# Kernel optimization log

Measured on AMD Instinct MI355X. Metric: run time of the kernel, lower is better.

## Reference

```python
import jax, jax.numpy as jnp
import numpy as np

B, N, DIM, C_IN, C_OUT = 2, 512, 3, 64, 64


def setup_inputs() -> dict:
    key = jax.random.key(0)
    ks = jax.random.split(key, 9)
    geom = jax.random.normal(ks[0], (B, N, DIM, C_IN), dtype=jnp.float32)
    adj = jax.random.uniform(ks[1], (B, N, N, 1, 1), dtype=jnp.float32)
    rel = jax.random.normal(ks[2], (B, N, N, DIM, 1), dtype=jnp.float32)
    emb = jax.random.normal(ks[3], (B, N, N, 1), dtype=jnp.float32)
    # learned parameters
    theta = jax.random.normal(ks[4], (C_IN + 1, C_OUT), dtype=jnp.float32) * 0.1
    norm_w = jax.random.normal(ks[5], (C_IN + 1, 1), dtype=jnp.float32) * 0.1
    norm_b = jax.random.normal(ks[6], (1,), dtype=jnp.float32) * 0.1
    alpha = jax.random.normal(ks[7], (1, 1, C_OUT), dtype=jnp.float32) * 0.1
    beta = jax.random.normal(ks[8], (1, 1, C_OUT), dtype=jnp.float32) * 0.1
    return {
        "geometric_information": geom,
        "adjacency_matrix": adj,
        "relative_point_cloud": rel,
        "embed_pc_and_features": emb,
        "theta": theta,
        "norm_w": norm_w,
        "norm_b": norm_b,
        "alpha": alpha,
        "beta": beta,
    }


def reference(geometric_information, adjacency_matrix, relative_point_cloud,
              embed_pc_and_features, theta, norm_w, norm_b, alpha, beta):
    b, n, d, c_in = geometric_information.shape
    # broadcast sender features to all pairs: [B,n,n,3,C_in]
    g2 = jnp.broadcast_to(geometric_information[:, None], (b, n, n, d, c_in))
    # concat relative coords as an extra channel: [B,n,n,3,C_in+1]
    embed_x_and_g = jnp.concatenate([g2, relative_point_cloud], axis=-1)
    # use_all_norms branch (block_id != 0): per-channel L2 norm over spatial axis
    norms = jnp.sqrt(jnp.sum(embed_x_and_g * embed_x_and_g, axis=-2))  # [B,n,n,C_in+1]
    norm_and_feature = norms @ norm_w + norm_b + embed_pc_and_features  # [B,n,n,1]
    # P_alpha_beta: affine + activation -> [B,n,n,C_out]
    p_alpha_beta = jax.nn.relu(alpha * norm_and_feature + beta)
    # channel mixing: [B,n,n,3,C_out]
    mixed = embed_x_and_g @ theta
    # adjacency-masked sum over neighbor axis -> [B,n,3,C_out]
    out = jnp.sum(mixed * p_alpha_beta[..., None, :] * adjacency_matrix, axis=2)
    return out
```

## Files before the change

### kernel.cpp

```cpp
#include <hip/hip_runtime.h>
#include <math.h>

#define WS_S   0
#define WS_GM4 1024

typedef unsigned int u32;

static __device__ __forceinline__ u32 bf16b(float x) {
    u32 u = __builtin_bit_cast(u32, x);
    return (u + 0x7FFFu + ((u >> 16) & 1u)) >> 16;
}

__global__ __launch_bounds__(256) void prep_kernel(
    const float* __restrict__ geom,
    const float* __restrict__ theta,
    const float* __restrict__ norm_w,
    const float* __restrict__ norm_b,
    float* __restrict__ s,
    float* __restrict__ gm4,
    float* __restrict__ out)
{
    const int bx  = blockIdx.x;
    const int tid = threadIdx.x;

    for (int k = tid; k < 384; k += 256)
        out[(size_t)bx * 384 + k] = 0.f;

    if (bx < 256) {
        const int sub  = tid >> 6;
        const int lane = tid & 63;
        const int bj   = bx * 4 + sub;
        __shared__ float g[4][192];
        const float* gb = geom + (size_t)bj * 192;
        g[sub][lane]       = gb[lane];
        g[sub][lane + 64]  = gb[lane + 64];
        g[sub][lane + 128] = gb[lane + 128];
        __syncthreads();

        {
            float g0 = g[sub][lane], g1 = g[sub][64 + lane], g2 = g[sub][128 + lane];
            float t = sqrtf(g0 * g0 + g1 * g1 + g2 * g2) * norm_w[lane];
            for (int off = 32; off > 0; off >>= 1) t += __shfl_down(t, off);
            if (lane == 0) s[bj] = t + norm_b[0];
        }

        float a0 = 0.f, a1 = 0.f, a2 = 0.f;
        for (int c = 0; c < 64; ++c) {
            float th = theta[c * 64 + lane];
            a0 = fmaf(g[sub][c],       th, a0);
            a1 = fmaf(g[sub][64 + c],  th, a1);
            a2 = fmaf(g[sub][128 + c], th, a2);
        }
        *reinterpret_cast<float4*>(gm4 + (size_t)bj * 256 + lane * 4) =
            make_float4(a0, a1, a2, 0.f);
    }
}

__global__ __launch_bounds__(512) void main_kernel(
    const float* __restrict__ adj,
    const float* __restrict__ rel,
    const float* __restrict__ emb,
    const float* __restrict__ s,
    const float* __restrict__ gm4,
    const float* __restrict__ theta,
    const float* __restrict__ norm_w,
    const float* __restrict__ alpha,
    const float* __restrict__ beta,
    float* __restrict__ out)
{
    const int bx   = blockIdx.x;
    const int jh   = bx & 1;
    const int iq   = (bx >> 1) & 127;
    const int b    = bx >> 8;
    const int tid  = threadIdx.x;
    const int lane = tid & 63;
    const int wv   = tid >> 6;
    const int bi0  = b * 512 + iq * 4;
    const int j0   = jh * 256;

    __shared__ uint4 pk_l[4][256];
    __shared__ float red[8][768];

    {
        const float nw64 = norm_w[64];
        #pragma unroll
        for (int u = 0; u < 2; ++u) {
            int t  = tid + u * 512;
            int il = t >> 8;
            int j  = t & 255;
            size_t p = (size_t)(bi0 + il) * 512 + j0 + j;
            const float* rp = rel + p * 3;
            float r0 = rp[0], r1 = rp[1], r2 = rp[2];
            float a   = adj[p];
            float naf = s[b * 512 + j0 + j]
                      + nw64 * sqrtf(r0 * r0 + r1 * r1 + r2 * r2) + emb[p];
            uint4 q;
            q.x = __builtin_bit_cast(u32, a * naf);
            q.y = __builtin_bit_cast(u32, a);
            q.z = bf16b(r0) | (bf16b(r1) << 16);
            q.w = bf16b(r2) << 16;
            pk_l[il][j] = q;
        }
    }
    __syncthreads();

    const float al  = alpha[lane];
    const float be  = beta[lane];
    const float t64 = theta[64 * 64 + lane];

    const float4* gmv =
        (const float4*)gm4 + ((size_t)(b * 512 + j0 + wv * 32)) * 64 + lane;

    float acc[4][3];
    #pragma unroll
    for (int il = 0; il < 4; ++il)
        acc[il][0] = acc[il][1] = acc[il][2] = 0.f;

    #pragma unroll 4
    for (int jj = 0; jj < 32; ++jj) {
        float4 g = gmv[(size_t)jj * 64];
        #pragma unroll
        for (int il = 0; il < 4; ++il) {
            uint4 q = pk_l[il][wv * 32 + jj];
            float an = __builtin_bit_cast(float, q.x);
            float av = __builtin_bit_cast(float, q.y);
            float r0 = __builtin_bit_cast(float, q.z << 16);
            float r1 = __builtin_bit_cast(float, q.z & 0xFFFF0000u);
            float r2 = __builtin_bit_cast(float, q.w);
            float w  = fmaxf(fmaf(al, an, be * av), 0.f);
            acc[il][0] = fmaf(w, fmaf(r0, t64, g.x), acc[il][0]);
            acc[il][1] = fmaf(w, fmaf(r1, t64, g.y), acc[il][1]);
            acc[il][2] = fmaf(w, fmaf(r2, t64, g.z), acc[il][2]);
        }
    }

    float* rw = &red[wv][lane];
    #pragma unroll
    for (int il = 0; il < 4; ++il) {
        rw[il * 192]       = acc[il][0];
        rw[il * 192 + 64]  = acc[il][1];
        rw[il * 192 + 128] = acc[il][2];
    }
    __syncthreads();

    for (int k = tid; k < 768; k += 512) {
        float v = 0.f;
        #pragma unroll
        for (int w8 = 0; w8 < 8; ++w8) v += red[w8][k];
        int il = k / 192, r = k - il * 192;
        atomicAdd(&out[(size_t)(bi0 + il) * 192 + r], v);
    }
}

extern "C" void kernel_launch(void* const* d_in, const int* in_sizes, int n_in,
                              void* d_out, int out_size, void* d_ws, size_t ws_size,
                              hipStream_t stream) {
    const float* geom   = (const float*)d_in[0];
    const float* adj    = (const float*)d_in[1];
    const float* rel    = (const float*)d_in[2];
    const float* emb    = (const float*)d_in[3];
    const float* theta  = (const float*)d_in[4];
    const float* norm_w = (const float*)d_in[5];
    const float* norm_b = (const float*)d_in[6];
    const float* alpha  = (const float*)d_in[7];
    const float* beta   = (const float*)d_in[8];
    float* out = (float*)d_out;

    float* ws  = (float*)d_ws;
    float* s   = ws + WS_S;
    float* gm4 = ws + WS_GM4;

    prep_kernel<<<512, 256, 0, stream>>>(geom, theta, norm_w, norm_b, s, gm4, out);
    main_kernel<<<512, 512, 0, stream>>>(adj, rel, emb, s, gm4, theta, norm_w,
                                         alpha, beta, out);
}
```

Measured before the change: 22.57 us.

## Precompute packed per-pair records in prep kernel and DMA them into LDS

```diff
diff --git a/kernel.cpp b/kernel.cpp
--- a/kernel.cpp
+++ b/kernel.cpp
@@ -3,28 +3,29 @@
 
 #define WS_S   0
 #define WS_GM4 1024
+#define WS_PK  (1024 + 262144)
 
 typedef unsigned int u32;
-
-static __device__ __forceinline__ u32 bf16b(float x) {
-    u32 u = __builtin_bit_cast(u32, x);
-    return (u + 0x7FFFu + ((u >> 16) & 1u)) >> 16;
-}
+typedef const __attribute__((address_space(1))) void g_void;
+typedef __attribute__((address_space(3))) void l_void;
 
 __global__ __launch_bounds__(256) void prep_kernel(
     const float* __restrict__ geom,
+    const float* __restrict__ adj,
+    const float* __restrict__ rel,
+    const float* __restrict__ emb,
     const float* __restrict__ theta,
     const float* __restrict__ norm_w,
     const float* __restrict__ norm_b,
     float* __restrict__ s,
     float* __restrict__ gm4,
+    uint4* __restrict__ pk,
     float* __restrict__ out)
 {
     const int bx  = blockIdx.x;
     const int tid = threadIdx.x;
 
-    for (int k = tid; k < 384; k += 256)
-        out[(size_t)bx * 384 + k] = 0.f;
+    if (bx < 1024 && tid < 192) out[(size_t)bx * 192 + tid] = 0.f;
 
     if (bx < 256) {
         const int sub  = tid >> 6;
@@ -53,17 +54,32 @@
         }
         *reinterpret_cast<float4*>(gm4 + (size_t)bj * 256 + lane * 4) =
             make_float4(a0, a1, a2, 0.f);
+    } else {
+        const int bi = bx - 256;
+        const float nw64 = norm_w[64];
+        #pragma unroll
+        for (int k = 0; k < 2; ++k) {
+            int j = tid + k * 256;
+            size_t p = (size_t)bi * 512 + j;
+            float r0 = rel[p * 3], r1 = rel[p * 3 + 1], r2 = rel[p * 3 + 2];
+            float e2 = fmaf(nw64, sqrtf(r0 * r0 + r1 * r1 + r2 * r2), emb[p]);
+            uint4 q;
+            q.x = __builtin_bit_cast(u32, e2);
+            q.y = __builtin_bit_cast(u32, adj[p]);
+            q.z = __builtin_amdgcn_perm(__builtin_bit_cast(u32, r1),
+                                        __builtin_bit_cast(u32, r0),
+                                        0x07060302u);
+            q.w = __builtin_bit_cast(u32, r2);
+            pk[p] = q;
+        }
     }
 }
 
 __global__ __launch_bounds__(512) void main_kernel(
-    const float* __restrict__ adj,
-    const float* __restrict__ rel,
-    const float* __restrict__ emb,
-    const float* __restrict__ s,
+    const uint4* __restrict__ pk,
+    const float* __restrict__ s_arr,
     const float* __restrict__ gm4,
     const float* __restrict__ theta,
-    const float* __restrict__ norm_w,
     const float* __restrict__ alpha,
     const float* __restrict__ beta,
     float* __restrict__ out)
@@ -79,29 +95,19 @@
     const int j0   = jh * 256;
 
     __shared__ uint4 pk_l[4][256];
+    __shared__ float s_l[256];
     __shared__ float red[8][768];
 
-    {
-        const float nw64 = norm_w[64];
-        #pragma unroll
-        for (int u = 0; u < 2; ++u) {
-            int t  = tid + u * 512;
-            int il = t >> 8;
-            int j  = t & 255;
-            size_t p = (size_t)(bi0 + il) * 512 + j0 + j;
-            const float* rp = rel + p * 3;
-            float r0 = rp[0], r1 = rp[1], r2 = rp[2];
-            float a   = adj[p];
-            float naf = s[b * 512 + j0 + j]
-                      + nw64 * sqrtf(r0 * r0 + r1 * r1 + r2 * r2) + emb[p];
-            uint4 q;
-            q.x = __builtin_bit_cast(u32, a * naf);
-            q.y = __builtin_bit_cast(u32, a);
-            q.z = bf16b(r0) | (bf16b(r1) << 16);
-            q.w = bf16b(r2) << 16;
-            pk_l[il][j] = q;
-        }
+    const uint4* srcbase = pk + (size_t)bi0 * 512 + j0;
+    #pragma unroll
+    for (int u = 0; u < 2; ++u) {
+        int unit = wv + u * 8;
+        int il = unit >> 2, jg = unit & 3;
+        __builtin_amdgcn_global_load_lds(
+            (g_void*)(srcbase + (size_t)il * 512 + jg * 64 + lane),
+            (l_void*)((char*)&pk_l[0][0] + unit * 1024), 16, 0, 0);
     }
+    if (tid < 256) s_l[tid] = s_arr[b * 512 + j0 + tid];
     __syncthreads();
 
     const float al  = alpha[lane];
@@ -118,16 +124,18 @@
 
     #pragma unroll 4
     for (int jj = 0; jj < 32; ++jj) {
-        float4 g = gmv[(size_t)jj * 64];
+        float4 g   = gmv[(size_t)jj * 64];
+        float  sj  = s_l[wv * 32 + jj];
+        float  bej = fmaf(al, sj, be);
         #pragma unroll
         for (int il = 0; il < 4; ++il) {
             uint4 q = pk_l[il][wv * 32 + jj];
-            float an = __builtin_bit_cast(float, q.x);
+            float e2 = __builtin_bit_cast(float, q.x);
             float av = __builtin_bit_cast(float, q.y);
             float r0 = __builtin_bit_cast(float, q.z << 16);
             float r1 = __builtin_bit_cast(float, q.z & 0xFFFF0000u);
             float r2 = __builtin_bit_cast(float, q.w);
-            float w  = fmaxf(fmaf(al, an, be * av), 0.f);
+            float w  = av * fmaxf(fmaf(al, e2, bej), 0.f);
             acc[il][0] = fmaf(w, fmaf(r0, t64, g.x), acc[il][0]);
             acc[il][1] = fmaf(w, fmaf(r1, t64, g.y), acc[il][1]);
             acc[il][2] = fmaf(w, fmaf(r2, t64, g.z), acc[il][2]);
@@ -169,8 +177,9 @@
     float* ws  = (float*)d_ws;
     float* s   = ws + WS_S;
     float* gm4 = ws + WS_GM4;
+    uint4* pk  = (uint4*)(ws + WS_PK);
 
-    prep_kernel<<<512, 256, 0, stream>>>(geom, theta, norm_w, norm_b, s, gm4, out);
-    main_kernel<<<512, 512, 0, stream>>>(adj, rel, emb, s, gm4, theta, norm_w,
-                                         alpha, beta, out);
+    prep_kernel<<<1280, 256, 0, stream>>>(geom, adj, rel, emb, theta, norm_w,
+                                          norm_b, s, gm4, pk, out);
+    main_kernel<<<512, 512, 0, stream>>>(pk, s, gm4, theta, alpha, beta, out);
 }
```

New measurement: 26.40 us. 1.17x slower.

## Keep per-pair edge data in registers and broadcast via readlane instead of LDS

Applied to the files above, without the earlier changes.

```diff
diff --git a/kernel.cpp b/kernel.cpp
--- a/kernel.cpp
+++ b/kernel.cpp
@@ -4,11 +4,9 @@
 #define WS_S   0
 #define WS_GM4 1024
 
-typedef unsigned int u32;
-
-static __device__ __forceinline__ u32 bf16b(float x) {
-    u32 u = __builtin_bit_cast(u32, x);
-    return (u + 0x7FFFu + ((u >> 16) & 1u)) >> 16;
+static __device__ __forceinline__ float rlf(float v, int l) {
+    return __builtin_bit_cast(float,
+        __builtin_amdgcn_readlane(__builtin_bit_cast(int, v), l));
 }
 
 __global__ __launch_bounds__(256) void prep_kernel(
@@ -60,7 +58,7 @@
     const float* __restrict__ adj,
     const float* __restrict__ rel,
     const float* __restrict__ emb,
-    const float* __restrict__ s,
+    const float* __restrict__ s_arr,
     const float* __restrict__ gm4,
     const float* __restrict__ theta,
     const float* __restrict__ norm_w,
@@ -78,31 +76,27 @@
     const int bi0  = b * 512 + iq * 4;
     const int j0   = jh * 256;
 
-    __shared__ uint4 pk_l[4][256];
-    __shared__ float red[8][768];
+    const int il_off = lane >> 5;
+    const int jp     = j0 + wv * 32 + (lane & 31);
+    const float nw64 = norm_w[64];
+    const float sj   = s_arr[b * 512 + jp];
 
+    float anA, avA, r0A, r1A, r2A;
+    float anB, avB, r0B, r1B, r2B;
     {
-        const float nw64 = norm_w[64];
-        #pragma unroll
-        for (int u = 0; u < 2; ++u) {
-            int t  = tid + u * 512;
-            int il = t >> 8;
-            int j  = t & 255;
-            size_t p = (size_t)(bi0 + il) * 512 + j0 + j;
-            const float* rp = rel + p * 3;
-            float r0 = rp[0], r1 = rp[1], r2 = rp[2];
-            float a   = adj[p];
-            float naf = s[b * 512 + j0 + j]
-                      + nw64 * sqrtf(r0 * r0 + r1 * r1 + r2 * r2) + emb[p];
-            uint4 q;
-            q.x = __builtin_bit_cast(u32, a * naf);
-            q.y = __builtin_bit_cast(u32, a);
-            q.z = bf16b(r0) | (bf16b(r1) << 16);
-            q.w = bf16b(r2) << 16;
-            pk_l[il][j] = q;
-        }
+        size_t p = (size_t)(bi0 + il_off) * 512 + jp;
+        r0A = rel[p * 3]; r1A = rel[p * 3 + 1]; r2A = rel[p * 3 + 2];
+        avA = adj[p];
+        float e2 = fmaf(nw64, sqrtf(r0A * r0A + r1A * r1A + r2A * r2A), emb[p]);
+        anA = avA * (sj + e2);
     }
-    __syncthreads();
+    {
+        size_t p = (size_t)(bi0 + il_off + 2) * 512 + jp;
+        r0B = rel[p * 3]; r1B = rel[p * 3 + 1]; r2B = rel[p * 3 + 2];
+        avB = adj[p];
+        float e2 = fmaf(nw64, sqrtf(r0B * r0B + r1B * r1B + r2B * r2B), emb[p]);
+        anB = avB * (sj + e2);
+    }
 
     const float al  = alpha[lane];
     const float be  = beta[lane];
@@ -116,24 +110,27 @@
     for (int il = 0; il < 4; ++il)
         acc[il][0] = acc[il][1] = acc[il][2] = 0.f;
 
-    #pragma unroll 4
+#define PAIR(AN, AV, R0, R1, R2, IDX, A0, A1, A2)                          \
+    {                                                                      \
+        float an = rlf(AN, IDX), av = rlf(AV, IDX);                        \
+        float r0 = rlf(R0, IDX), r1 = rlf(R1, IDX), r2 = rlf(R2, IDX);     \
+        float w  = fmaxf(fmaf(al, an, be * av), 0.f);                      \
+        A0 = fmaf(w, fmaf(r0, t64, g.x), A0);                              \
+        A1 = fmaf(w, fmaf(r1, t64, g.y), A1);                              \
+        A2 = fmaf(w, fmaf(r2, t64, g.z), A2);                              \
+    }
+
+    #pragma unroll
     for (int jj = 0; jj < 32; ++jj) {
         float4 g = gmv[(size_t)jj * 64];
-        #pragma unroll
-        for (int il = 0; il < 4; ++il) {
-            uint4 q = pk_l[il][wv * 32 + jj];
-            float an = __builtin_bit_cast(float, q.x);
-            float av = __builtin_bit_cast(float, q.y);
-            float r0 = __builtin_bit_cast(float, q.z << 16);
-            float r1 = __builtin_bit_cast(float, q.z & 0xFFFF0000u);
-            float r2 = __builtin_bit_cast(float, q.w);
-            float w  = fmaxf(fmaf(al, an, be * av), 0.f);
-            acc[il][0] = fmaf(w, fmaf(r0, t64, g.x), acc[il][0]);
-            acc[il][1] = fmaf(w, fmaf(r1, t64, g.y), acc[il][1]);
-            acc[il][2] = fmaf(w, fmaf(r2, t64, g.z), acc[il][2]);
-        }
+        PAIR(anA, avA, r0A, r1A, r2A, jj,      acc[0][0], acc[0][1], acc[0][2]);
+        PAIR(anA, avA, r0A, r1A, r2A, 32 + jj, acc[1][0], acc[1][1], acc[1][2]);
+        PAIR(anB, avB, r0B, r1B, r2B, jj,      acc[2][0], acc[2][1], acc[2][2]);
+        PAIR(anB, avB, r0B, r1B, r2B, 32 + jj, acc[3][0], acc[3][1], acc[3][2]);
     }
+#undef PAIR
 
+    __shared__ float red[8][768];
     float* rw = &red[wv][lane];
     #pragma unroll
     for (int il = 0; il < 4; ++il) {
```

Measured after the change: 26.78 us. +18.7%, slower.
